# Kernel optimization log

Hardware: AMD Instinct MI355X
Metric: run time of the kernel (lower is better)

## Reference

```python
import jax, jax.numpy as jnp
import numpy as np
from jax.scipy.special import gammaln

WARMUP = 365
KERNEL = 15
PRECISION = 1e-5

# [lo, hi] per parameter, order: BETA FC K0 K1 K2 LP PERC UZL TT CFMAX CFR CWH A THETA
PARAM_RANGES = np.array([
    [1.0, 6.0], [50.0, 1000.0], [0.05, 0.9], [0.01, 0.5], [0.001, 0.2],
    [0.2, 1.0], [0.0, 10.0], [0.0, 100.0], [-2.5, 2.5], [0.5, 10.0],
    [0.0, 0.1], [0.0, 0.2], [0.0, 2.9], [0.0, 6.5],
], dtype=np.float32)


def scale_params(parameters):
    lo = jnp.asarray(PARAM_RANGES[:, 0])
    hi = jnp.asarray(PARAM_RANGES[:, 1])
    return lo + parameters * (hi - lo)  # [n_grid, 14]


def run_hbv(p_all, pet_all, t_all, phys, init_state):
    beta, fc, k0, k1, k2 = phys[:, 0], phys[:, 1], phys[:, 2], phys[:, 3], phys[:, 4]
    lp, pperc, uzl, tt = phys[:, 5], phys[:, 6], phys[:, 7], phys[:, 8]
    cfmax, cfr, cwh = phys[:, 9], phys[:, 10], phys[:, 11]

    def step(state, inp):
        snowpack, meltwater, sm, suz, slz = state
        precip, potent, tempre = inp
        is_rain = (tempre >= tt).astype(jnp.float32)
        rain = precip * is_rain
        snow = precip * (1.0 - is_rain)
        snowpack = snowpack + snow
        melt = jnp.minimum(jnp.maximum(cfmax * (tempre - tt), 0.0), snowpack)
        meltwater = meltwater + melt
        snowpack = snowpack - melt
        refreezing = jnp.minimum(jnp.maximum(cfr * cfmax * (tt - tempre), 0.0), meltwater)
        snowpack = snowpack + refreezing
        meltwater = meltwater - refreezing
        to_soil = jnp.maximum(meltwater - cwh * snowpack, 0.0)
        meltwater = meltwater - to_soil
        soil_wetness = jnp.clip((sm / fc) ** beta, 0.0, 1.0)
        recharge = (rain + to_soil) * soil_wetness
        sm = sm + rain + to_soil - recharge
        excess = jnp.maximum(sm - fc, 0.0)
        sm = sm - excess
        evap_factor = jnp.clip(sm / (lp * fc), 0.0, 1.0)
        et_act = jnp.minimum(sm, potent * evap_factor)
        sm = jnp.maximum(sm - et_act, PRECISION)
        suz = suz + recharge + excess
        perc = jnp.minimum(suz, pperc)
        suz = suz - perc
        q0 = k0 * jnp.maximum(suz - uzl, 0.0)
        suz = suz - q0
        q1 = k1 * suz
        suz = suz - q1
        slz = slz + perc
        q2 = k2 * slz
        slz = slz - q2
        return (snowpack, meltwater, sm, suz, slz), q0 + q1 + q2

    final_state, q_sim = jax.lax.scan(step, init_state, (p_all, pet_all, t_all))
    return q_sim, final_state


def uh_gamma(a, b, len_uh):
    # a, b: [n_grid]; returns normalized gamma-pdf unit hydrograph [len_uh, n_grid]
    aa = jax.nn.relu(a) + 0.1
    theta = jax.nn.relu(b) + 0.5
    t = jnp.arange(0.5, len_uh, dtype=jnp.float32)[:, None]  # [K, 1]
    log_w = (aa - 1.0) * jnp.log(t) - t / theta - gammaln(aa) - aa * jnp.log(theta)
    w = jnp.exp(log_w)
    return w / w.sum(axis=0, keepdims=True)


def hbv_forward(x, parameters):
    n_grid = x.shape[1]
    phys = scale_params(parameters)
    init = tuple(jnp.full((n_grid,), 0.001, dtype=jnp.float32) for _ in range(5))
    # warmup under no_grad -> stop_gradient on resulting states
    xw = x[:WARMUP]
    _, warm_state = run_hbv(xw[..., 0], xw[..., 1], xw[..., 2], phys, init)
    warm_state = jax.lax.stop_gradient(warm_state)
    xm = x[WARMUP:]
    q_sim, _ = run_hbv(xm[..., 0], xm[..., 1], xm[..., 2], phys, warm_state)  # [n_step, n_grid]
    # gamma unit-hydrograph routing (causal conv over time, per grid cell)
    uh = uh_gamma(phys[:, 12], phys[:, 13], KERNEL)  # [K, n_grid]
    n_step = q_sim.shape[0]
    qp = jnp.pad(q_sim, ((KERNEL - 1, 0), (0, 0)))
    qs = jnp.zeros_like(q_sim)
    for k in range(KERNEL):
        qs = qs + uh[k] * jax.lax.dynamic_slice_in_dim(qp, KERNEL - 1 - k, n_step, 0)
    return qs[..., None]  # [n_step, n_grid, 1]


def setup_inputs() -> dict:
    key = jax.random.key(0)
    k1, k2, k3, k4 = jax.random.split(key, 4)
    T, G = 2190, 10000  # 365 warmup + 1825 simulated days, 10k basins
    precip = jax.random.uniform(k1, (T, G), dtype=jnp.float32) * 10.0  # mm/day
    pet = jax.random.uniform(k2, (T, G), dtype=jnp.float32) * 5.0      # mm/day
    temp = jax.random.normal(k3, (T, G), dtype=jnp.float32) * 10.0     # deg C
    x = jnp.stack([precip, pet, temp], axis=-1)
    parameters = jax.random.uniform(k4, (G, 14), dtype=jnp.float32)
    return {"x": x, "parameters": parameters}


def reference(x, parameters):
    return hbv_forward(x, parameters)
```

## Files before the change

### kernel.cpp

```cpp
#include <hip/hip_runtime.h>

#define WARMUP  365
#define NSTEP   1825
#define TTOT    2190
#define KERNEL_ 15
#define CH      5

__global__ __launch_bounds__(64) void hbv_fused_kernel(
    const float* __restrict__ x,
    const float* __restrict__ params,
    float* __restrict__ out,
    int G)
{
    const int g = blockIdx.x * 64 + threadIdx.x;
    if (g >= G) return;

    const float* pr = params + (size_t)g * 14;
    const float beta  = 1.0f   + pr[0]  * 5.0f;
    const float fc    = 50.0f  + pr[1]  * 950.0f;
    const float k0    = 0.05f  + pr[2]  * 0.85f;
    const float k1    = 0.01f  + pr[3]  * 0.49f;
    const float k2    = 0.001f + pr[4]  * 0.199f;
    const float lp    = 0.2f   + pr[5]  * 0.8f;
    const float pperc =          pr[6]  * 10.0f;
    const float uzl   =          pr[7]  * 100.0f;
    const float tt    = -2.5f  + pr[8]  * 5.0f;
    const float cfmax = 0.5f   + pr[9]  * 9.5f;
    const float cfr   =          pr[10] * 0.1f;
    const float cwh   =          pr[11] * 0.2f;
    const float ra    =          pr[12] * 2.9f;
    const float rb    =          pr[13] * 6.5f;

    const float aa = fmaxf(ra, 0.0f) + 0.1f;
    const float th = fmaxf(rb, 0.0f) + 0.5f;
    const float inv_th = 1.0f / th;
    float w[KERNEL_];
    float ws = 0.0f;
    #pragma unroll
    for (int k = 0; k < KERNEL_; k++) {
        const float tk = 0.5f + (float)k;
        const float lw = (aa - 1.0f) * __logf(tk) - tk * inv_th;
        w[k] = __expf(lw);
        ws += w[k];
    }
    const float inv_ws = 1.0f / ws;
    #pragma unroll
    for (int k = 0; k < KERNEL_; k++) w[k] *= inv_ws;

    const float inv_fc   = 1.0f / fc;
    const float inv_lpfc = 1.0f / (lp * fc);
    const float cfrx     = cfr * cfmax;

    float sp  = 0.001f;
    float mw  = 0.001f;
    float sm  = 0.001f;
    float suz = 0.001f;
    float slz = 0.001f;

    auto step = [&](float precip, float pet, float temp) -> float {
        const float rain = (temp >= tt) ? precip : 0.0f;
        const float snow = precip - rain;
        sp += snow;
        const float melt = fminf(fmaxf(cfmax * (temp - tt), 0.0f), sp);
        mw += melt;
        sp -= melt;
        const float refr = fminf(fmaxf(cfrx * (tt - temp), 0.0f), mw);
        sp += refr;
        mw -= refr;
        const float tosoil = fmaxf(mw - cwh * sp, 0.0f);
        mw -= tosoil;
        const float r   = sm * inv_fc;
        float wet = __expf(beta * __logf(r));
        wet = fminf(wet, 1.0f);
        const float inflow = rain + tosoil;
        const float rech   = inflow * wet;
        sm += inflow - rech;
        const float exc = fmaxf(sm - fc, 0.0f);
        sm -= exc;
        const float ef = fminf(sm * inv_lpfc, 1.0f);
        const float et = fminf(sm, pet * ef);
        sm = fmaxf(sm - et, 1e-5f);
        suz += rech + exc;
        const float perc = fminf(suz, pperc);
        suz -= perc;
        const float q0 = k0 * fmaxf(suz - uzl, 0.0f);
        suz -= q0;
        const float q1 = k1 * suz;
        suz -= q1;
        slz += perc;
        const float q2 = k2 * slz;
        slz -= q2;
        return q0 + q1 + q2;
    };

    float cur[CH][3];
    #pragma unroll
    for (int i = 0; i < CH; i++) {
        const float* p = x + ((size_t)i * G + g) * 3;
        cur[i][0] = p[0]; cur[i][1] = p[1]; cur[i][2] = p[2];
    }

    for (int tc = 0; tc < WARMUP; tc += CH) {
        float nxt[CH][3];
        #pragma unroll
        for (int i = 0; i < CH; i++) {
            const float* p = x + ((size_t)(tc + CH + i) * G + g) * 3;
            nxt[i][0] = p[0]; nxt[i][1] = p[1]; nxt[i][2] = p[2];
        }
        #pragma unroll
        for (int i = 0; i < CH; i++)
            (void)step(cur[i][0], cur[i][1], cur[i][2]);
        #pragma unroll
        for (int i = 0; i < CH; i++) {
            cur[i][0] = nxt[i][0]; cur[i][1] = nxt[i][1]; cur[i][2] = nxt[i][2];
        }
    }

    float buf[KERNEL_];
    #pragma unroll
    for (int k = 0; k < KERNEL_; k++) buf[k] = 0.0f;

    for (int tc = WARMUP; tc < TTOT; tc += CH) {
        float nxt[CH][3];
        #pragma unroll
        for (int i = 0; i < CH; i++) {
            int tn = tc + CH + i;
            if (tn > TTOT - 1) tn = TTOT - 1;
            const float* p = x + ((size_t)tn * G + g) * 3;
            nxt[i][0] = p[0]; nxt[i][1] = p[1]; nxt[i][2] = p[2];
        }
        #pragma unroll
        for (int i = 0; i < CH; i++) {
            const float q = step(cur[i][0], cur[i][1], cur[i][2]);
            #pragma unroll
            for (int k = KERNEL_ - 1; k > 0; k--) buf[k] = buf[k - 1];
            buf[0] = q;
            float acc = 0.0f;
            #pragma unroll
            for (int k = 0; k < KERNEL_; k++) acc = fmaf(w[k], buf[k], acc);
            out[(size_t)(tc - WARMUP + i) * G + g] = acc;
        }
        #pragma unroll
        for (int i = 0; i < CH; i++) {
            cur[i][0] = nxt[i][0]; cur[i][1] = nxt[i][1]; cur[i][2] = nxt[i][2];
        }
    }
}

extern "C" void kernel_launch(void* const* d_in, const int* in_sizes, int n_in,
                              void* d_out, int out_size, void* d_ws, size_t ws_size,
                              hipStream_t stream) {
    const float* x      = (const float*)d_in[0];
    const float* params = (const float*)d_in[1];
    float* out = (float*)d_out;
    const int G = in_sizes[1] / 14;
    const int blocks = (G + 63) / 64;
    hbv_fused_kernel<<<blocks, 64, 0, stream>>>(x, params, out, G);
}
```

Measured before the change: 660.8 us.

## Prefetch 15-step input groups and use circular UH buffer with nontemporal stores

Raises the software prefetch depth from 5 to 15 timesteps per group, so more global loads are in flight while the serial recurrence runs. The shift-register convolution buffer becomes a compile-time circular index aligned to the group size, which removes the register moves done every step. Outputs are written with nontemporal stores. The price is more registers for the doubled 15x3 input arrays, which could lower occupancy, plus hand-coded group counts tied to the fixed sequence lengths.

Result: slower. 1.138 ms (+72.3%).

```diff
diff --git a/kernel.cpp b/kernel.cpp
--- a/kernel.cpp
+++ b/kernel.cpp
@@ -4,7 +4,7 @@
 #define NSTEP   1825
 #define TTOT    2190
 #define KERNEL_ 15
-#define CH      5
+#define GRP     15
 
 __global__ __launch_bounds__(64) void hbv_fused_kernel(
     const float* __restrict__ x,
@@ -58,20 +58,19 @@
     float slz = 0.001f;
 
     auto step = [&](float precip, float pet, float temp) -> float {
-        const float rain = (temp >= tt) ? precip : 0.0f;
-        const float snow = precip - rain;
-        sp += snow;
-        const float melt = fminf(fmaxf(cfmax * (temp - tt), 0.0f), sp);
+        const float dt   = temp - tt;
+        const float rain = (dt >= 0.0f) ? precip : 0.0f;
+        sp += precip - rain;
+        const float melt = fminf(fmaxf(cfmax * dt, 0.0f), sp);
         mw += melt;
         sp -= melt;
-        const float refr = fminf(fmaxf(cfrx * (tt - temp), 0.0f), mw);
+        const float refr = fminf(fmaxf(-cfrx * dt, 0.0f), mw);
         sp += refr;
         mw -= refr;
         const float tosoil = fmaxf(mw - cwh * sp, 0.0f);
         mw -= tosoil;
         const float r   = sm * inv_fc;
-        float wet = __expf(beta * __logf(r));
-        wet = fminf(wet, 1.0f);
+        const float wet = fminf(__expf(beta * __logf(r)), 1.0f);
         const float inflow = rain + tosoil;
         const float rech   = inflow * wet;
         sm += inflow - rech;
@@ -93,57 +92,69 @@
         return q0 + q1 + q2;
     };
 
-    float cur[CH][3];
-    #pragma unroll
-    for (int i = 0; i < CH; i++) {
-        const float* p = x + ((size_t)i * G + g) * 3;
-        cur[i][0] = p[0]; cur[i][1] = p[1]; cur[i][2] = p[2];
-    }
+    float cur[GRP][3], nxt[GRP][3];
 
-    for (int tc = 0; tc < WARMUP; tc += CH) {
-        float nxt[CH][3];
+    auto loadg = [&](int t0, float (&dst)[GRP][3]) {
         #pragma unroll
-        for (int i = 0; i < CH; i++) {
-            const float* p = x + ((size_t)(tc + CH + i) * G + g) * 3;
-            nxt[i][0] = p[0]; nxt[i][1] = p[1]; nxt[i][2] = p[2];
+        for (int j = 0; j < GRP; j++) {
+            int t = t0 + j;
+            if (t > TTOT - 1) t = TTOT - 1;
+            const float* p = x + ((size_t)t * G + g) * 3;
+            dst[j][0] = p[0]; dst[j][1] = p[1]; dst[j][2] = p[2];
         }
+    };
+    auto advance = [&]() {
         #pragma unroll
-        for (int i = 0; i < CH; i++)
-            (void)step(cur[i][0], cur[i][1], cur[i][2]);
-        #pragma unroll
-        for (int i = 0; i < CH; i++) {
-            cur[i][0] = nxt[i][0]; cur[i][1] = nxt[i][1]; cur[i][2] = nxt[i][2];
+        for (int j = 0; j < GRP; j++) {
+            cur[j][0] = nxt[j][0]; cur[j][1] = nxt[j][1]; cur[j][2] = nxt[j][2];
         }
-    }
+    };
 
     float buf[KERNEL_];
     #pragma unroll
     for (int k = 0; k < KERNEL_; k++) buf[k] = 0.0f;
 
-    for (int tc = WARMUP; tc < TTOT; tc += CH) {
-        float nxt[CH][3];
+    loadg(0, cur);
+
+    for (int grp = 0; grp < 24; ++grp) {
+        loadg(grp * GRP + GRP, nxt);
         #pragma unroll
-        for (int i = 0; i < CH; i++) {
-            int tn = tc + CH + i;
-            if (tn > TTOT - 1) tn = TTOT - 1;
-            const float* p = x + ((size_t)tn * G + g) * 3;
-            nxt[i][0] = p[0]; nxt[i][1] = p[1]; nxt[i][2] = p[2];
-        }
+        for (int j = 0; j < GRP; j++)
+            (void)step(cur[j][0], cur[j][1], cur[j][2]);
+        advance();
+    }
+    loadg(375, nxt);
+    #pragma unroll
+    for (int j = 0; j < 5; j++)
+        (void)step(cur[j][0], cur[j][1], cur[j][2]);
+    #pragma unroll
+    for (int j = 0; j < 10; j++) {
+        const float q = step(cur[5 + j][0], cur[5 + j][1], cur[5 + j][2]);
+        buf[j] = q;
+        float acc = 0.0f;
         #pragma unroll
-        for (int i = 0; i < CH; i++) {
-            const float q = step(cur[i][0], cur[i][1], cur[i][2]);
-            #pragma unroll
-            for (int k = KERNEL_ - 1; k > 0; k--) buf[k] = buf[k - 1];
-            buf[0] = q;
+        for (int k = 0; k < KERNEL_; k++)
+            acc = fmaf(w[k], buf[(j - k + KERNEL_) % KERNEL_], acc);
+        __builtin_nontemporal_store(acc, out + (size_t)j * G + g);
+    }
+    advance();
+
+    for (int grp = 0; grp < 121; ++grp) {
+        const int t0 = 375 + grp * GRP;
+        const int m0 = t0 - WARMUP;
+        loadg(t0 + GRP, nxt);
+        #pragma unroll
+        for (int j = 0; j < GRP; j++) {
+            const float q = step(cur[j][0], cur[j][1], cur[j][2]);
+            const int p = (10 + j) % KERNEL_;
+            buf[p] = q;
             float acc = 0.0f;
             #pragma unroll
-            for (int k = 0; k < KERNEL_; k++) acc = fmaf(w[k], buf[k], acc);
-            out[(size_t)(tc - WARMUP + i) * G + g] = acc;
+            for (int k = 0; k < KERNEL_; k++)
+                acc = fmaf(w[k], buf[(p - k + KERNEL_) % KERNEL_], acc);
+            __builtin_nontemporal_store(acc, out + (size_t)(m0 + j) * G + g);
         }
-        #pragma unroll
-        for (int i = 0; i < CH; i++) {
-            cur[i][0] = nxt[i][0]; cur[i][1] = nxt[i][1]; cur[i][2] = nxt[i][2];
-        }
+        advance();
     }
 }
 
```
